# Kernel tuning notes

Hardware: AMD Instinct MI355X
Metric: run time of the kernel (lower is better)

Reference implementation:

```python
import jax, jax.numpy as jnp
import numpy as np

IN_DIM, OUT_DIM = 32, 16
NUM_BINS, EMBED, HEADS = 1100, 8, 4
MN, MX = -1.0, 300.0
BATCH = 1024


def setup_inputs() -> dict:
    key = jax.random.key(0)
    ks = jax.random.split(key, 8)
    s = 1.0 / np.sqrt(EMBED)
    x = jax.random.uniform(ks[0], (BATCH, IN_DIM), jnp.float32, MN, MX)
    emb = jax.random.normal(ks[1], (IN_DIM, NUM_BINS, EMBED), jnp.float32)  # per-feature tables
    in_proj_w = jax.random.uniform(ks[2], (3 * EMBED, EMBED), jnp.float32, -s, s)
    in_proj_b = jnp.zeros((3 * EMBED,), jnp.float32)
    out_proj_w = jax.random.uniform(ks[3], (EMBED, EMBED), jnp.float32, -s, s)
    out_proj_b = jnp.zeros((EMBED,), jnp.float32)
    sl = 1.0 / np.sqrt(IN_DIM * EMBED)
    lin_w = jax.random.uniform(ks[4], (OUT_DIM, IN_DIM * EMBED), jnp.float32, -sl, sl)
    lin_b = jax.random.uniform(ks[5], (OUT_DIM,), jnp.float32, -sl, sl)
    return {"x": x, "emb": emb, "in_proj_w": in_proj_w, "in_proj_b": in_proj_b,
            "out_proj_w": out_proj_w, "out_proj_b": out_proj_b,
            "lin_w": lin_w, "lin_b": lin_b}


def reference(x, emb, in_proj_w, in_proj_b, out_proj_w, out_proj_b, lin_w, lin_b):
    B, F = x.shape
    H, hd = HEADS, EMBED // HEADS
    # clamp + bucketize (torch.bucketize right=False == searchsorted side='left')
    bins = jnp.linspace(MN, MX, NUM_BINS)
    idx = jnp.searchsorted(bins, jnp.clip(x, MN, MX), side="left")  # (B, F)
    # per-feature embedding gather
    xe = emb[jnp.arange(F)[None, :], idx]  # (B, F, E)
    # MultiheadAttention with batch_first=False: seq axis = B, batch axis = F
    Wq, Wk, Wv = jnp.split(in_proj_w, 3, axis=0)
    bq, bk, bv = jnp.split(in_proj_b, 3)
    q = (xe @ Wq.T + bq).reshape(B, F, H, hd)
    k = (xe @ Wk.T + bk).reshape(B, F, H, hd)
    v = (xe @ Wv.T + bv).reshape(B, F, H, hd)
    scores = jnp.einsum("bfhd,cfhd->fhbc", q, k) / np.sqrt(hd)  # (F, H, B, B)
    attn = jax.nn.softmax(scores, axis=-1)
    o = jnp.einsum("fhbc,cfhd->bfhd", attn, v).reshape(B, F, EMBED)
    o = o @ out_proj_w.T + out_proj_b  # (B, F, E)
    logits = o.reshape(B, F * EMBED) @ lin_w.T + lin_b  # (B, OUT_DIM)
    return jax.nn.softmax(logits, axis=-1)
```

## Files before the change

### kernel.cpp

```cpp
#include <hip/hip_runtime.h>
#include <math.h>

#define NF 32
#define NB 1100
#define NE 8
#define NH 4
#define NBATCH 1024
#define NFH 128

__device__ __forceinline__ float fexp2(float x){
#if __has_builtin(__builtin_amdgcn_exp2f)
  return __builtin_amdgcn_exp2f(x);
#else
  return exp2f(x);
#endif
}

__device__ __forceinline__ double bin_at(int i){
  #pragma clang fp contract(off)
  const double step = 301.0 / 1099.0;
  if (i == NB - 1) return 300.0;
  return (double)i * step + (-1.0);
}

__global__ __launch_bounds__(256) void k1_embed_qkv(
    const float* __restrict__ x, const float* __restrict__ emb,
    const float* __restrict__ W, const float* __restrict__ bias,
    float* __restrict__ q_ws, float* __restrict__ kv_ws)
{
  __shared__ float sW[192];
  __shared__ float sB[24];
  const int tid = threadIdx.x;
  if (tid < 192) sW[tid] = W[tid];
  if (tid < 24)  sB[tid] = bias[tid];
  __syncthreads();

  const int f = blockIdx.y;
  const int b = blockIdx.x * 256 + tid;

  float xv = x[b * NF + f];
  xv = fminf(fmaxf(xv, -1.0f), 300.0f);
  const double xd = (double)xv;

  int lo = 0, hi = NB;
  while (lo < hi) {
    const int mid = (lo + hi) >> 1;
    if (bin_at(mid) < xd) lo = mid + 1; else hi = mid;
  }
  const int idx = lo;

  const float4* ep = (const float4*)(emb + ((size_t)f * NB + idx) * NE);
  const float4 e0 = ep[0], e1 = ep[1];
  const float xe[8] = {e0.x, e0.y, e0.z, e0.w, e1.x, e1.y, e1.z, e1.w};

  float qv[8], kv[8], vv[8];
  #pragma unroll
  for (int i = 0; i < 8; ++i) { qv[i] = sB[i]; kv[i] = sB[8+i]; vv[i] = sB[16+i]; }
  #pragma unroll
  for (int j = 0; j < 8; ++j) {
    const float xj = xe[j];
    #pragma unroll
    for (int i = 0; i < 8; ++i) {
      qv[i] = fmaf(xj, sW[      i*8 + j], qv[i]);
      kv[i] = fmaf(xj, sW[ 64 + i*8 + j], kv[i]);
      vv[i] = fmaf(xj, sW[128 + i*8 + j], vv[i]);
    }
  }

  const float QS = (float)(1.4426950408889634 / 1.4142135623730951);
  float2* qp = (float2*)q_ws;
  float4* kvp = (float4*)kv_ws;
  #pragma unroll
  for (int h = 0; h < NH; ++h) {
    const int fh = f * NH + h;
    qp [fh * NBATCH + b] = make_float2(qv[2*h] * QS, qv[2*h+1] * QS);
    kvp[fh * NBATCH + b] = make_float4(kv[2*h], kv[2*h+1], vv[2*h], vv[2*h+1]);
  }
}

__global__ __launch_bounds__(256) void k2_attn(
    const float* __restrict__ q_ws, const float* __restrict__ kv_ws,
    float* __restrict__ o_ws)
{
  __shared__ float4 skv[NBATCH];
  __shared__ float sred[4];
  const int tid = threadIdx.x;
  const int fh = blockIdx.y;

  const float4* kvg = (const float4*)kv_ws + (size_t)fh * NBATCH;
  float mx2 = 0.0f;
  #pragma unroll
  for (int i = 0; i < 4; ++i) {
    const float4 t = kvg[i * 256 + tid];
    skv[i * 256 + tid] = t;
    mx2 = fmaxf(mx2, fmaf(t.x, t.x, t.y * t.y));
  }
  #pragma unroll
  for (int off = 32; off >= 1; off >>= 1)
    mx2 = fmaxf(mx2, __shfl_xor(mx2, off, 64));
  if ((tid & 63) == 0) sred[tid >> 6] = mx2;
  __syncthreads();
  const float Mn = sqrtf(fmaxf(fmaxf(sred[0], sred[1]), fmaxf(sred[2], sred[3])));

  const int b = blockIdx.x * 256 + tid;
  const float2 q = ((const float2*)q_ws)[(size_t)fh * NBATCH + b];
  const float m = sqrtf(fmaf(q.x, q.x, q.y * q.y)) * Mn;

  float l = 0.0f, o0 = 0.0f, o1 = 0.0f;
  #pragma unroll 4
  for (int c = 0; c < NBATCH; ++c) {
    const float4 kv = skv[c];
    const float s = fmaf(q.x, kv.x, fmaf(q.y, kv.y, -m));
    const float p = fexp2(s);
    l += p;
    o0 = fmaf(p, kv.z, o0);
    o1 = fmaf(p, kv.w, o1);
  }
  const float inv = 1.0f / l;
  ((float2*)o_ws)[(size_t)fh * NBATCH + b] = make_float2(o0 * inv, o1 * inv);
}

__global__ void k_comb(const float* __restrict__ opw, const float* __restrict__ opb,
                       const float* __restrict__ lw,  const float* __restrict__ lb,
                       float* __restrict__ Wcomb, float* __restrict__ bcomb)
{
  __shared__ float sWo[64];
  const int tid = threadIdx.x;
  if (tid < 64) sWo[tid] = opw[tid];
  __syncthreads();
  for (int i = tid; i < 4096; i += 256) {
    const int t = i >> 8, fe = i & 255;
    const int f8 = fe & ~7, e2 = fe & 7;
    float acc = 0.0f;
    #pragma unroll
    for (int e = 0; e < 8; ++e) acc = fmaf(lw[t*256 + f8 + e], sWo[e*8 + e2], acc);
    Wcomb[i] = acc;
  }
  if (tid < 16) {
    float acc = lb[tid];
    for (int fe = 0; fe < 256; ++fe) acc = fmaf(lw[tid*256 + fe], opb[fe & 7], acc);
    bcomb[tid] = acc;
  }
}

__global__ __launch_bounds__(256) void k3_final(
    const float* __restrict__ o_ws, const float* __restrict__ Wcomb,
    const float* __restrict__ bcomb, float* __restrict__ out)
{
  const int gid = blockIdx.x * 256 + threadIdx.x;
  const int b = gid >> 4;
  const int t = gid & 15;
  const float2* op = (const float2*)o_ws;
  const float2* wp = (const float2*)Wcomb + t * 128;
  float acc = bcomb[t];
  #pragma unroll 8
  for (int fh = 0; fh < NFH; ++fh) {
    const float2 ov = op[(size_t)fh * NBATCH + b];
    const float2 wv = wp[fh];
    acc = fmaf(ov.x, wv.x, fmaf(ov.y, wv.y, acc));
  }
  float mx = acc;
  #pragma unroll
  for (int off = 8; off >= 1; off >>= 1) mx = fmaxf(mx, __shfl_xor(mx, off, 64));
  const float p = expf(acc - mx);
  float s = p;
  #pragma unroll
  for (int off = 8; off >= 1; off >>= 1) s += __shfl_xor(s, off, 64);
  out[gid] = p / s;
}

extern "C" void kernel_launch(void* const* d_in, const int* in_sizes, int n_in,
                              void* d_out, int out_size, void* d_ws, size_t ws_size,
                              hipStream_t stream)
{
  const float* x   = (const float*)d_in[0];
  const float* emb = (const float*)d_in[1];
  const float* ipw = (const float*)d_in[2];
  const float* ipb = (const float*)d_in[3];
  const float* opw = (const float*)d_in[4];
  const float* opb = (const float*)d_in[5];
  const float* lw  = (const float*)d_in[6];
  const float* lb  = (const float*)d_in[7];

  float* ws    = (float*)d_ws;
  float* q_ws  = ws;
  float* kv_ws = ws + 262144;
  float* o_ws  = ws + 786432;
  float* Wcomb = ws + 1048576;
  float* bcomb = ws + 1052672;

  k1_embed_qkv<<<dim3(4, NF), 256, 0, stream>>>(x, emb, ipw, ipb, q_ws, kv_ws);
  k_comb<<<1, 256, 0, stream>>>(opw, opb, lw, lb, Wcomb, bcomb);
  k2_attn<<<dim3(4, NFH), 256, 0, stream>>>(q_ws, kv_ws, o_ws);
  k3_final<<<64, 256, 0, stream>>>(o_ws, Wcomb, bcomb, (float*)d_out);
}
```

Before: 125.1 us.

## Split attention key range across two thread halves and fuse weight-combine into final kernel

```diff
diff --git a/kernel.cpp b/kernel.cpp
--- a/kernel.cpp
+++ b/kernel.cpp
@@ -78,81 +78,97 @@
   }
 }
 
-__global__ __launch_bounds__(256) void k2_attn(
+__global__ __launch_bounds__(512) void k2_attn(
     const float* __restrict__ q_ws, const float* __restrict__ kv_ws,
     float* __restrict__ o_ws)
 {
   __shared__ float4 skv[NBATCH];
-  __shared__ float sred[4];
+  __shared__ float sred[8];
+  __shared__ float sl[256], so0[256], so1[256];
   const int tid = threadIdx.x;
   const int fh = blockIdx.y;
 
   const float4* kvg = (const float4*)kv_ws + (size_t)fh * NBATCH;
-  float mx2 = 0.0f;
-  #pragma unroll
-  for (int i = 0; i < 4; ++i) {
-    const float4 t = kvg[i * 256 + tid];
-    skv[i * 256 + tid] = t;
-    mx2 = fmaxf(mx2, fmaf(t.x, t.x, t.y * t.y));
-  }
+  const float4 t0 = kvg[tid], t1 = kvg[tid + 512];
+  skv[tid] = t0;
+  skv[tid + 512] = t1;
+  float mx2 = fmaxf(fmaf(t0.x, t0.x, t0.y * t0.y), fmaf(t1.x, t1.x, t1.y * t1.y));
   #pragma unroll
   for (int off = 32; off >= 1; off >>= 1)
     mx2 = fmaxf(mx2, __shfl_xor(mx2, off, 64));
   if ((tid & 63) == 0) sred[tid >> 6] = mx2;
   __syncthreads();
-  const float Mn = sqrtf(fmaxf(fmaxf(sred[0], sred[1]), fmaxf(sred[2], sred[3])));
-
-  const int b = blockIdx.x * 256 + tid;
+  float Mn2 = sred[0];
+  #pragma unroll
+  for (int w = 1; w < 8; ++w) Mn2 = fmaxf(Mn2, sred[w]);
+  const float Mn = sqrtf(Mn2);
+
+  const int qi = tid & 255;
+  const int half = tid >> 8;
+  const int b = blockIdx.x * 256 + qi;
   const float2 q = ((const float2*)q_ws)[(size_t)fh * NBATCH + b];
-  const float m = sqrtf(fmaf(q.x, q.x, q.y * q.y)) * Mn;
+  const float negm = -sqrtf(fmaf(q.x, q.x, q.y * q.y)) * Mn;
 
   float l = 0.0f, o0 = 0.0f, o1 = 0.0f;
-  #pragma unroll 4
-  for (int c = 0; c < NBATCH; ++c) {
-    const float4 kv = skv[c];
-    const float s = fmaf(q.x, kv.x, fmaf(q.y, kv.y, -m));
+  const int c0 = half << 9;
+  #pragma unroll 8
+  for (int c = 0; c < 512; ++c) {
+    const float4 kv = skv[c0 + c];
+    const float s = fmaf(q.x, kv.x, fmaf(q.y, kv.y, negm));
     const float p = fexp2(s);
     l += p;
     o0 = fmaf(p, kv.z, o0);
     o1 = fmaf(p, kv.w, o1);
   }
-  const float inv = 1.0f / l;
-  ((float2*)o_ws)[(size_t)fh * NBATCH + b] = make_float2(o0 * inv, o1 * inv);
-}
-
-__global__ void k_comb(const float* __restrict__ opw, const float* __restrict__ opb,
-                       const float* __restrict__ lw,  const float* __restrict__ lb,
-                       float* __restrict__ Wcomb, float* __restrict__ bcomb)
-{
+  if (half == 1) { sl[qi] = l; so0[qi] = o0; so1[qi] = o1; }
+  __syncthreads();
+  if (half == 0) {
+    l += sl[qi]; o0 += so0[qi]; o1 += so1[qi];
+    const float inv = 1.0f / l;
+    ((float2*)o_ws)[(size_t)fh * NBATCH + b] = make_float2(o0 * inv, o1 * inv);
+  }
+}
+
+__global__ __launch_bounds__(256) void k3_final(
+    const float* __restrict__ o_ws, const float* __restrict__ opw,
+    const float* __restrict__ opb,  const float* __restrict__ lw,
+    const float* __restrict__ lb,   float* __restrict__ out)
+{
+  __shared__ float sWc[4096];
+  __shared__ float sbc[16];
   __shared__ float sWo[64];
   const int tid = threadIdx.x;
   if (tid < 64) sWo[tid] = opw[tid];
   __syncthreads();
+  #pragma unroll
   for (int i = tid; i < 4096; i += 256) {
     const int t = i >> 8, fe = i & 255;
     const int f8 = fe & ~7, e2 = fe & 7;
     float acc = 0.0f;
     #pragma unroll
     for (int e = 0; e < 8; ++e) acc = fmaf(lw[t*256 + f8 + e], sWo[e*8 + e2], acc);
-    Wcomb[i] = acc;
-  }
-  if (tid < 16) {
-    float acc = lb[tid];
-    for (int fe = 0; fe < 256; ++fe) acc = fmaf(lw[tid*256 + fe], opb[fe & 7], acc);
-    bcomb[tid] = acc;
-  }
-}
-
-__global__ __launch_bounds__(256) void k3_final(
-    const float* __restrict__ o_ws, const float* __restrict__ Wcomb,
-    const float* __restrict__ bcomb, float* __restrict__ out)
-{
-  const int gid = blockIdx.x * 256 + threadIdx.x;
+    sWc[i] = acc;
+  }
+  {
+    const int t = tid >> 4, seg = tid & 15;
+    float acc = 0.0f;
+    #pragma unroll
+    for (int j = 0; j < 16; ++j) {
+      const int fe = seg * 16 + j;
+      acc = fmaf(lw[t*256 + fe], opb[fe & 7], acc);
+    }
+    #pragma unroll
+    for (int off = 8; off >= 1; off >>= 1) acc += __shfl_xor(acc, off, 64);
+    if (seg == 0) sbc[t] = acc + lb[t];
+  }
+  __syncthreads();
+
+  const int gid = blockIdx.x * 256 + tid;
   const int b = gid >> 4;
   const int t = gid & 15;
   const float2* op = (const float2*)o_ws;
-  const float2* wp = (const float2*)Wcomb + t * 128;
-  float acc = bcomb[t];
+  const float2* wp = (const float2*)sWc + t * 128;
+  float acc = sbc[t];
   #pragma unroll 8
   for (int fh = 0; fh < NFH; ++fh) {
     const float2 ov = op[(size_t)fh * NBATCH + b];
@@ -186,11 +202,8 @@
   float* q_ws  = ws;
   float* kv_ws = ws + 262144;
   float* o_ws  = ws + 786432;
-  float* Wcomb = ws + 1048576;
-  float* bcomb = ws + 1052672;
 
   k1_embed_qkv<<<dim3(4, NF), 256, 0, stream>>>(x, emb, ipw, ipb, q_ws, kv_ws);
-  k_comb<<<1, 256, 0, stream>>>(opw, opb, lw, lb, Wcomb, bcomb);
-  k2_attn<<<dim3(4, NFH), 256, 0, stream>>>(q_ws, kv_ws, o_ws);
-  k3_final<<<64, 256, 0, stream>>>(o_ws, Wcomb, bcomb, (float*)d_out);
-}
+  k2_attn<<<dim3(4, NFH), 512, 0, stream>>>(q_ws, kv_ws, o_ws);
+  k3_final<<<64, 256, 0, stream>>>(o_ws, opw, opb, lw, lb, (float*)d_out);
+}
```

Result: faster. 109.7 us (-12.3%).
